# Optimization experiments

Measured on AMD Instinct MI355X. Metric: run time of the kernel, lower is better.

The kernel has to match this reference:

```python
import jax, jax.numpy as jnp
import numpy as np

B, C, H, W, K = 4, 64, 128, 128, 3
K2 = K * K
PAD = (K - 1) // 2  # same padding for 3x3


def setup_inputs() -> dict:
    key = jax.random.key(0)
    ks = jax.random.split(key, 9)
    s = 0.05
    return {
        "x": jax.random.normal(ks[0], (B, C, H, W), jnp.float32),
        "inter": jax.random.normal(ks[1], (B, C, H, W), jnp.float32),
        # offset/mask predictor conv: input cat([x, inter]) -> 3*K2 channels (dy, dx, mask)
        "w_offset": jax.random.normal(ks[2], (3 * K2, 2 * C, K, K), jnp.float32) * s,
        "b_offset": jnp.zeros((3 * K2,), jnp.float32),
        # deformable conv weight (bias=False per DGM init)
        "w_dcn": jax.random.normal(ks[3], (C, C, K, K), jnp.float32) * s,
        # SFT gamma branch: two 1x1 convs (bias=False)
        "w_g1": jax.random.normal(ks[4], (C, C), jnp.float32) * s,
        "w_g2": jax.random.normal(ks[5], (C, C), jnp.float32) * s,
        # SFT beta branch: two 1x1 convs (bias=False)
        "w_b1": jax.random.normal(ks[6], (C, C), jnp.float32) * s,
        "w_b2": jax.random.normal(ks[7], (C, C), jnp.float32) * s,
    }


def _lrelu(v):
    # LeakyReLU(0.1)
    return jnp.where(v >= 0, v, 0.1 * v)


def _conv(x, w, b=None):
    y = jax.lax.conv_general_dilated(
        x, w, window_strides=(1, 1), padding=[(PAD, PAD), (PAD, PAD)],
        dimension_numbers=("NCHW", "OIHW", "NCHW"))
    if b is not None:
        y = y + b[None, :, None, None]
    return y


def _bilinear_gather(x, py, px):
    """x: [B,C,H,W]; py, px: [B,K2,H,W] float sample coords.
    Returns samples [B,K2,H,W,C]; out-of-bounds treated as zero (DCN zero-pad)."""
    y0 = jnp.floor(py)
    x0 = jnp.floor(px)
    wy = (py - y0)[..., None]
    wx = (px - x0)[..., None]

    def gather(yi, xi):
        valid = ((yi >= 0) & (yi < H) & (xi >= 0) & (xi < W)).astype(x.dtype)
        yc = jnp.clip(yi, 0, H - 1).astype(jnp.int32)
        xc = jnp.clip(xi, 0, W - 1).astype(jnp.int32)
        bidx = jnp.arange(B)[:, None, None, None]
        v = x[bidx, :, yc, xc]  # advanced indexing -> [B,K2,H,W,C]
        return v * valid[..., None]

    v00 = gather(y0, x0)
    v01 = gather(y0, x0 + 1)
    v10 = gather(y0 + 1, x0)
    v11 = gather(y0 + 1, x0 + 1)
    return (v00 * (1 - wy) * (1 - wx) + v01 * (1 - wy) * wx
            + v10 * wy * (1 - wx) + v11 * wy * wx)


def _dgm_forward(x, inter, w_offset, b_offset, w_dcn, w_g1, w_g2, w_b1, w_b2):
    # --- WADCN branch: modulated deformable conv, offsets predicted from cat(x, inter)
    om = _conv(jnp.concatenate([x, inter], axis=1), w_offset, b_offset)  # [B,3K2,H,W]
    dy, dx, m = jnp.split(om, 3, axis=1)  # each [B,K2,H,W]
    mask = jax.nn.sigmoid(m)

    ky, kx = jnp.meshgrid(jnp.arange(K), jnp.arange(K), indexing="ij")
    ky = ky.reshape(K2).astype(x.dtype)
    kx = kx.reshape(K2).astype(x.dtype)
    hh = jnp.arange(H, dtype=x.dtype)
    ww = jnp.arange(W, dtype=x.dtype)
    # sample coords: base grid + kernel-tap offset + learned offset
    py = hh[None, None, :, None] + (ky - PAD)[None, :, None, None] + dy  # [B,K2,H,W]
    px = ww[None, None, None, :] + (kx - PAD)[None, :, None, None] + dx

    samp = _bilinear_gather(x, py, px) * mask[..., None]  # [B,K2,H,W,C]
    dcn_out = jnp.einsum("bkhwc,ock->bohw", samp, w_dcn.reshape(C, C, K2))

    # --- SFT branch: two 1x1-conv + LeakyReLU chains producing gamma/beta
    gamma = jnp.einsum("oc,bchw->bohw", w_g2,
                       _lrelu(jnp.einsum("oc,bchw->bohw", w_g1, inter)))
    beta = jnp.einsum("oc,bchw->bohw", w_b2,
                      _lrelu(jnp.einsum("oc,bchw->bohw", w_b1, inter)))
    sft_out = x * gamma + beta

    # --- fused residual combine (DGM.relu is defined but never applied)
    return x + dcn_out + sft_out


def reference(x, inter, w_offset, b_offset, w_dcn, w_g1, w_g2, w_b1, w_b2):
    return _dgm_forward(x, inter, w_offset, b_offset, w_dcn, w_g1, w_g2, w_b1, w_b2)
```

## Files before the change

kernel.cpp:

```cpp
#include <hip/hip_runtime.h>
#include <hip/hip_bf16.h>
#include <math.h>

#define BB 4
#define CC 64
#define HH 128
#define WW 128
#define HW (HH*WW)
#define NPIX (BB*HW)

typedef __attribute__((ext_vector_type(8))) short short8;
typedef __attribute__((ext_vector_type(4))) float f32x4;

__device__ __forceinline__ float bf2f(ushort u) {
  union { unsigned u; float f; } v; v.u = ((unsigned)u) << 16; return v.f;
}
__device__ __forceinline__ ushort f2bf(float f) {
  __hip_bfloat16 h = __float2bfloat16(f); return *(ushort*)&h;
}

#define XOFS   0u
#define IOFS   4194304u
#define ZPOFS  12017664u

__global__ __launch_bounds__(256) void k_transp(
    const float* __restrict__ x, const float* __restrict__ inter,
    ushort* __restrict__ x_clh, ushort* __restrict__ inter_clh) {
  __shared__ float tile[64 * 129];
  int blk = blockIdx.x;
  int sel = blk >> 9;
  int bh = blk & 511;
  int b = bh >> 7, h = bh & 127;
  const float* src = sel ? inter : x;
  ushort* dst = sel ? inter_clh : x_clh;
  const float* sp = src + (size_t)(b * 64) * HW + h * WW;
  for (int i = threadIdx.x; i < 64 * 128; i += 256) {
    int c = i >> 7, w = i & 127;
    tile[c * 129 + w] = sp[(size_t)c * HW + w];
  }
  __syncthreads();
  ushort* dp = dst + ((size_t)b * HW + h * WW) * 64;
  for (int i = threadIdx.x; i < 64 * 128; i += 256) {
    int w = i >> 6, c = i & 63;
    dp[w * 64 + c] = f2bf(tile[c * 129 + w]);
  }
}

__global__ void k_wprep(const float* __restrict__ w_off,
                        const float* __restrict__ w_dcn,
                        const float* __restrict__ wg1, const float* __restrict__ wb1,
                        const float* __restrict__ wg2, const float* __restrict__ wb2,
                        ushort* __restrict__ wfb, ushort* __restrict__ wdT,
                        ushort* __restrict__ w1gb, ushort* __restrict__ w1bb,
                        ushort* __restrict__ w2gb, ushort* __restrict__ w2bb,
                        float* __restrict__ zp) {
  int blk = blockIdx.x;
  if (blk < 144) {
    int i = blk * 256 + threadIdx.x;
    if (i < 64) zp[i] = 0.f;
    if (i < 9 * 32 * 128) {
      int tap = i >> 12, rem = i & 4095, m = rem >> 7, c = rem & 127;
      float v = (m < 27) ? w_off[(size_t)(m * 128 + c) * 9 + tap] : 0.f;
      wfb[i] = f2bf(v);
    }
  } else if (blk < 288) {
    int i = (blk - 144) * 256 + threadIdx.x;
    if (i < 64 * 64 * 9) {
      int o = i / 576, rem = i % 576, k = rem >> 6, c = rem & 63;
      wdT[i] = f2bf(w_dcn[(o * 64 + c) * 9 + k]);
    }
  } else {
    int i = (blk - 288) * 256 + threadIdx.x;
    int m = i >> 12, j = i & 4095;
    const float* src = (m == 0) ? wg1 : (m == 1) ? wb1 : (m == 2) ? wg2 : wb2;
    ushort* dst = (m == 0) ? w1gb : (m == 1) ? w1bb : (m == 2) ? w2gb : w2bb;
    dst[j] = f2bf(src[j]);
  }
}

#define FPITCH 72

__global__ __launch_bounds__(256) void k_sft(
    const float* __restrict__ x, const ushort* __restrict__ inter_clh,
    const ushort* __restrict__ w1gb, const ushort* __restrict__ w1bb,
    const ushort* __restrict__ w2gb, const ushort* __restrict__ w2bb,
    float* __restrict__ out) {
  __shared__ ushort Sg[64 * FPITCH];
  __shared__ ushort Sb[64 * FPITCH];
  int tid = threadIdx.x;
  int lane = tid & 63;
  int quad = lane >> 4, col = lane & 15;
  int pg0 = blockIdx.x * 64;
  int b = pg0 >> 14, hw0 = pg0 & 16383;
  int o_base = __builtin_amdgcn_readfirstlane((tid >> 6) * 16);

  f32x4 ag[4], ab[4];
#pragma unroll
  for (int nt = 0; nt < 4; ++nt) {
    ag[nt] = (f32x4){0.f, 0.f, 0.f, 0.f};
    ab[nt] = (f32x4){0.f, 0.f, 0.f, 0.f};
  }
#pragma unroll
  for (int ks = 0; ks < 2; ++ks) {
    short8 a_g = *(const short8*)(w1gb + (size_t)(o_base + col) * 64 + ks * 32 + quad * 8);
    short8 a_b = *(const short8*)(w1bb + (size_t)(o_base + col) * 64 + ks * 32 + quad * 8);
#pragma unroll
    for (int nt = 0; nt < 4; ++nt) {
      short8 bf = *(const short8*)(inter_clh + (size_t)(pg0 + nt * 16 + col) * 64 + ks * 32 + quad * 8);
      ag[nt] = __builtin_amdgcn_mfma_f32_16x16x32_bf16(a_g, bf, ag[nt], 0, 0, 0);
      ab[nt] = __builtin_amdgcn_mfma_f32_16x16x32_bf16(a_b, bf, ab[nt], 0, 0, 0);
    }
  }
#pragma unroll
  for (int nt = 0; nt < 4; ++nt) {
    int px = nt * 16 + col;
    ushort pkg[4], pkb[4];
#pragma unroll
    for (int r = 0; r < 4; ++r) {
      float vg = ag[nt][r]; vg = vg >= 0.f ? vg : 0.1f * vg;
      float vb = ab[nt][r]; vb = vb >= 0.f ? vb : 0.1f * vb;
      pkg[r] = f2bf(vg); pkb[r] = f2bf(vb);
    }
    *(uint2*)(&Sg[px * FPITCH + o_base + quad * 4]) = *(uint2*)pkg;
    *(uint2*)(&Sb[px * FPITCH + o_base + quad * 4]) = *(uint2*)pkb;
  }
  __syncthreads();

  f32x4 gg[4], gb[4];
#pragma unroll
  for (int nt = 0; nt < 4; ++nt) {
    gg[nt] = (f32x4){0.f, 0.f, 0.f, 0.f};
    gb[nt] = (f32x4){0.f, 0.f, 0.f, 0.f};
  }
#pragma unroll
  for (int ks = 0; ks < 2; ++ks) {
    short8 a_g = *(const short8*)(w2gb + (size_t)(o_base + col) * 64 + ks * 32 + quad * 8);
    short8 a_b = *(const short8*)(w2bb + (size_t)(o_base + col) * 64 + ks * 32 + quad * 8);
#pragma unroll
    for (int nt = 0; nt < 4; ++nt) {
      short8 bg = *(const short8*)(Sg + (nt * 16 + col) * FPITCH + ks * 32 + quad * 8);
      short8 bb = *(const short8*)(Sb + (nt * 16 + col) * FPITCH + ks * 32 + quad * 8);
      gg[nt] = __builtin_amdgcn_mfma_f32_16x16x32_bf16(a_g, bg, gg[nt], 0, 0, 0);
      gb[nt] = __builtin_amdgcn_mfma_f32_16x16x32_bf16(a_b, bb, gb[nt], 0, 0, 0);
    }
  }

#pragma unroll
  for (int nt = 0; nt < 4; ++nt) {
#pragma unroll
    for (int r = 0; r < 4; ++r) {
      int o = o_base + quad * 4 + r;
      size_t idx = (size_t)(b * 64 + o) * HW + hw0 + nt * 16 + col;
      float xv = x[idx];
      out[idx] = xv + xv * gg[nt][r] + gb[nt][r];
    }
  }
}

__global__ __launch_bounds__(256, 2) void k_convm(
    const ushort* __restrict__ wsb, const ushort* __restrict__ wfb,
    float* __restrict__ om) {
  int tid = threadIdx.x;
  int wave = tid >> 6, lane = tid & 63;
  int quad = lane >> 4, col = lane & 15;
  int blk = blockIdx.x;
  int b = blk >> 7, h = blk & 127;
  int half = wave >> 1, mt = wave & 1;

  short8 A[36];
  {
    const ushort* wb0 = wfb + (size_t)(mt * 16 + col) * 128 + quad * 8;
#pragma unroll
    for (int tap = 0; tap < 9; ++tap)
#pragma unroll
      for (int g = 0; g < 2; ++g)
#pragma unroll
        for (int ks = 0; ks < 2; ++ks)
          A[tap * 4 + g * 2 + ks] =
              *(const short8*)(wb0 + (size_t)tap * 4096 + g * 64 + ks * 32);
  }

  unsigned bslab = (unsigned)b * HW * 64;
  int pgrow = b * HW + h * WW;

#pragma unroll 1
  for (int t = 0; t < 4; ++t) {
    int px = half * 64 + t * 16 + col;
    unsigned ofs[9];
#pragma unroll
    for (int ky = 0; ky < 3; ++ky) {
      int hs = h + ky - 1;
      bool hok = (unsigned)hs < 128u;
#pragma unroll
      for (int kx = 0; kx < 3; ++kx) {
        int ps = px + kx - 1;
        bool ok = hok && ((unsigned)ps < 128u);
        unsigned o = bslab + (unsigned)((hs << 7) + ps) * 64 + quad * 8;
        ofs[ky * 3 + kx] = ok ? o : ZPOFS;
      }
    }
    f32x4 accx = {0.f, 0.f, 0.f, 0.f}, acci = {0.f, 0.f, 0.f, 0.f};
#pragma unroll
    for (int tap = 0; tap < 9; ++tap) {
      const ushort* p = wsb + ofs[tap];
      short8 bx0 = *(const short8*)(p + XOFS);
      short8 bx1 = *(const short8*)(p + XOFS + 32);
      short8 bi0 = *(const short8*)(p + IOFS);
      short8 bi1 = *(const short8*)(p + IOFS + 32);
      accx = __builtin_amdgcn_mfma_f32_16x16x32_bf16(A[tap * 4 + 0], bx0, accx, 0, 0, 0);
      accx = __builtin_amdgcn_mfma_f32_16x16x32_bf16(A[tap * 4 + 1], bx1, accx, 0, 0, 0);
      acci = __builtin_amdgcn_mfma_f32_16x16x32_bf16(A[tap * 4 + 2], bi0, acci, 0, 0, 0);
      acci = __builtin_amdgcn_mfma_f32_16x16x32_bf16(A[tap * 4 + 3], bi1, acci, 0, 0, 0);
    }
    int pg = pgrow + px;
#pragma unroll
    for (int r = 0; r < 4; ++r) {
      int o = mt * 16 + quad * 4 + r;
      float v = accx[r] + acci[r];
      if (o < 27) om[(size_t)o * NPIX + pg] = v;
    }
  }
}

#define SPITCH 200
#define NPX 32

__global__ __launch_bounds__(256) void k_dcn(
    const ushort* __restrict__ x_clh, const float* __restrict__ om,
    const float* __restrict__ b_off, const ushort* __restrict__ wdT,
    const ushort* __restrict__ zp16,
    float* __restrict__ out) {
  __shared__ ushort S[NPX * SPITCH];
  __shared__ int   cy[9 * NPX], cx[9 * NPX];
  __shared__ float cwy[9 * NPX], cwx[9 * NPX], cm[9 * NPX];

  int tid = threadIdx.x;
  int wave = tid >> 6, lane = tid & 63;
  int quad = lane >> 4, col = lane & 15;
  int rr = lane >> 3, g = lane & 7;
  int pg0 = blockIdx.x * NPX;
  int b = pg0 >> 14;
  int o_base = __builtin_amdgcn_readfirstlane(wave * 16);

  for (int i = tid; i < 9 * NPX; i += 256) {
    int k = i >> 5, p = i & 31;
    int pg = pg0 + p;
    int hw = pg & 16383;
    int h = hw >> 7, w = hw & 127;
    float dy = om[(size_t)k * NPIX + pg] + b_off[k];
    float dx = om[(size_t)(9 + k) * NPIX + pg] + b_off[9 + k];
    float mz = om[(size_t)(18 + k) * NPIX + pg] + b_off[18 + k];
    float py = (float)(h + (k / 3) - 1) + dy;
    float px = (float)(w + (k % 3) - 1) + dx;
    float y0f = floorf(py), x0f = floorf(px);
    cy[i] = (int)y0f;
    cx[i] = (int)x0f;
    cwy[i] = py - y0f;
    cwx[i] = px - x0f;
    cm[i] = 1.f / (1.f + __expf(-mz));
  }

  f32x4 acc[2];
  acc[0] = (f32x4){0.f, 0.f, 0.f, 0.f};
  acc[1] = (f32x4){0.f, 0.f, 0.f, 0.f};

  const ushort* bp = x_clh + (size_t)b * HW * 64;

  for (int chunk = 0; chunk < 3; ++chunk) {
    __syncthreads();
#pragma unroll
    for (int it = 0; it < 3; ++it) {
      int p = wave * 8 + rr;
      int idx = (chunk * 3 + it) * NPX + p;
      int y0 = cy[idx], x0 = cx[idx];
      float wy = cwy[idx], wx = cwx[idx], m = cm[idx];
      bool yok0 = (unsigned)y0 < 128u, yok1 = (unsigned)(y0 + 1) < 128u;
      bool xok0 = (unsigned)x0 < 128u, xok1 = (unsigned)(x0 + 1) < 128u;
      const ushort* r0 = bp + ((size_t)(int)((y0 << 7) + x0)) * 64 + g * 8;
      const ushort* r1 = r0 + (size_t)WW * 64;
      short8 s00 = *(const short8*)((yok0 && xok0) ? r0 : zp16);
      short8 s01 = *(const short8*)((yok0 && xok1) ? (r0 + 64) : zp16);
      short8 s10 = *(const short8*)((yok1 && xok0) ? r1 : zp16);
      short8 s11 = *(const short8*)((yok1 && xok1) ? (r1 + 64) : zp16);
      short8 outv;
#pragma unroll
      for (int j = 0; j < 8; ++j) {
        float v00 = bf2f((ushort)s00[j]), v01 = bf2f((ushort)s01[j]);
        float v10 = bf2f((ushort)s10[j]), v11 = bf2f((ushort)s11[j]);
        float top = v00 + (v01 - v00) * wx;
        float bot = v10 + (v11 - v10) * wx;
        float val = top + (bot - top) * wy;
        outv[j] = (short)f2bf(val * m);
      }
      *(short8*)(&S[p * SPITCH + it * 64 + g * 8]) = outv;
    }
    __syncthreads();
    const ushort* wrow = wdT + (size_t)(o_base + col) * 576 + chunk * 192 + quad * 8;
    const ushort* srow = S + quad * 8;
#pragma unroll
    for (int ks = 0; ks < 6; ++ks) {
      short8 a = *(const short8*)(wrow + ks * 32);
#pragma unroll
      for (int nt = 0; nt < 2; ++nt) {
        short8 bf = *(const short8*)(srow + (nt * 16 + col) * SPITCH + ks * 32);
        acc[nt] = __builtin_amdgcn_mfma_f32_16x16x32_bf16(a, bf, acc[nt], 0, 0, 0);
      }
    }
  }

  int hw0 = pg0 & 16383;
#pragma unroll
  for (int nt = 0; nt < 2; ++nt) {
#pragma unroll
    for (int r = 0; r < 4; ++r) {
      int o = o_base + quad * 4 + r;
      size_t idx = (size_t)(b * 64 + o) * HW + hw0 + nt * 16 + col;
      out[idx] += acc[nt][r];
    }
  }
}

extern "C" void kernel_launch(void* const* d_in, const int* in_sizes, int n_in,
                              void* d_out, int out_size, void* d_ws, size_t ws_size,
                              hipStream_t stream) {
  const float* x     = (const float*)d_in[0];
  const float* inter = (const float*)d_in[1];
  const float* w_off = (const float*)d_in[2];
  const float* b_off = (const float*)d_in[3];
  const float* w_dcn = (const float*)d_in[4];
  const float* wg1   = (const float*)d_in[5];
  const float* wg2   = (const float*)d_in[6];
  const float* wb1   = (const float*)d_in[7];
  const float* wb2   = (const float*)d_in[8];
  float* out = (float*)d_out;

  float* ws        = (float*)d_ws;
  ushort* wsb      = (ushort*)d_ws;
  ushort* x_clh    = (ushort*)ws;
  ushort* inter_clh= (ushort*)(ws + 2097152);
  float* om        = ws + 4194304;
  ushort* wfb      = (ushort*)(ws + 5963776);
  ushort* wdT      = (ushort*)(ws + 5982208);
  ushort* w1gb     = (ushort*)(ws + 6000640);
  ushort* w1bb     = (ushort*)(ws + 6002688);
  ushort* w2gb     = (ushort*)(ws + 6004736);
  ushort* w2bb     = (ushort*)(ws + 6006784);
  float* zp        = ws + 6008832;

  k_transp<<<1024, 256, 0, stream>>>(x, inter, x_clh, inter_clh);
  k_wprep<<<352, 256, 0, stream>>>(w_off, w_dcn, wg1, wb1, wg2, wb2,
                                   wfb, wdT, w1gb, w1bb, w2gb, w2bb, zp);

  k_sft<<<1024, 256, 0, stream>>>(x, inter_clh, w1gb, w1bb, w2gb, w2bb, out);

  k_convm<<<512, 256, 0, stream>>>(wsb, wfb, om);

  k_dcn<<<2048, 256, 0, stream>>>(x_clh, om, b_off, wdT, (const ushort*)zp, out);
}
```

Measured before the change: 183.7 us.

## Split offset conv across more blocks and software-pipeline weight and input loads

The offset/mask conv kernel no longer preloads all 36 weight fragments into registers. Instead it streams each tap's weights and inputs, double-buffered one tap ahead. Each block now handles a quarter of an image row (32 pixels), one tile per wave, with 4x as many blocks and launch bounds raised to 4 blocks per CU. This lowers register pressure, raises occupancy and parallelism, and overlaps loads with MFMA. The cost is that weights are re-read from global/L2 for every pixel tile instead of once per block.

Result: slower. 206.6 us (+12.5%).

```diff
diff --git a/kernel.cpp b/kernel.cpp
--- a/kernel.cpp
+++ b/kernel.cpp
@@ -157,68 +157,78 @@
   }
 }
 
-__global__ __launch_bounds__(256, 2) void k_convm(
+__global__ __launch_bounds__(256, 4) void k_convm(
     const ushort* __restrict__ wsb, const ushort* __restrict__ wfb,
     float* __restrict__ om) {
   int tid = threadIdx.x;
   int wave = tid >> 6, lane = tid & 63;
   int quad = lane >> 4, col = lane & 15;
   int blk = blockIdx.x;
-  int b = blk >> 7, h = blk & 127;
-  int half = wave >> 1, mt = wave & 1;
-
-  short8 A[36];
+  int b = blk >> 9, h = (blk >> 2) & 127, wq = blk & 3;
+  int pt = wave >> 1, mt = wave & 1;
+  int px = wq * 32 + pt * 16 + col;
+
+  unsigned bslab = (unsigned)b * HW * 64;
+  unsigned ofsx[9], ofsi[9];
+#pragma unroll
+  for (int ky = 0; ky < 3; ++ky) {
+    int hs = h + ky - 1;
+    bool hok = (unsigned)hs < 128u;
+#pragma unroll
+    for (int kx = 0; kx < 3; ++kx) {
+      int ps = px + kx - 1;
+      bool ok = hok && ((unsigned)ps < 128u);
+      unsigned o = bslab + (unsigned)((hs << 7) + ps) * 64 + quad * 8;
+      ofsx[ky * 3 + kx] = ok ? (XOFS + o) : ZPOFS;
+      ofsi[ky * 3 + kx] = ok ? (IOFS + o) : ZPOFS;
+    }
+  }
+
+  const ushort* wb0 = wfb + (size_t)(mt * 16 + col) * 128 + quad * 8;
+
+  short8 bx0[2], bx1[2], bi0[2], bi1[2], a0[2], a1[2], a2[2], a3[2];
   {
-    const ushort* wb0 = wfb + (size_t)(mt * 16 + col) * 128 + quad * 8;
-#pragma unroll
-    for (int tap = 0; tap < 9; ++tap)
-#pragma unroll
-      for (int g = 0; g < 2; ++g)
-#pragma unroll
-        for (int ks = 0; ks < 2; ++ks)
-          A[tap * 4 + g * 2 + ks] =
-              *(const short8*)(wb0 + (size_t)tap * 4096 + g * 64 + ks * 32);
-  }
-
-  unsigned bslab = (unsigned)b * HW * 64;
-  int pgrow = b * HW + h * WW;
-
-#pragma unroll 1
-  for (int t = 0; t < 4; ++t) {
-    int px = half * 64 + t * 16 + col;
-    unsigned ofs[9];
-#pragma unroll
-    for (int ky = 0; ky < 3; ++ky) {
-      int hs = h + ky - 1;
-      bool hok = (unsigned)hs < 128u;
-#pragma unroll
-      for (int kx = 0; kx < 3; ++kx) {
-        int ps = px + kx - 1;
-        bool ok = hok && ((unsigned)ps < 128u);
-        unsigned o = bslab + (unsigned)((hs << 7) + ps) * 64 + quad * 8;
-        ofs[ky * 3 + kx] = ok ? o : ZPOFS;
-      }
-    }
-    f32x4 accx = {0.f, 0.f, 0.f, 0.f}, acci = {0.f, 0.f, 0.f, 0.f};
-#pragma unroll
-    for (int tap = 0; tap < 9; ++tap) {
-      const ushort* p = wsb + ofs[tap];
-      short8 bx0 = *(const short8*)(p + XOFS);
-      short8 bx1 = *(const short8*)(p + XOFS + 32);
-      short8 bi0 = *(const short8*)(p + IOFS);
-      short8 bi1 = *(const short8*)(p + IOFS + 32);
-      accx = __builtin_amdgcn_mfma_f32_16x16x32_bf16(A[tap * 4 + 0], bx0, accx, 0, 0, 0);
-      accx = __builtin_amdgcn_mfma_f32_16x16x32_bf16(A[tap * 4 + 1], bx1, accx, 0, 0, 0);
-      acci = __builtin_amdgcn_mfma_f32_16x16x32_bf16(A[tap * 4 + 2], bi0, acci, 0, 0, 0);
-      acci = __builtin_amdgcn_mfma_f32_16x16x32_bf16(A[tap * 4 + 3], bi1, acci, 0, 0, 0);
-    }
-    int pg = pgrow + px;
-#pragma unroll
-    for (int r = 0; r < 4; ++r) {
-      int o = mt * 16 + quad * 4 + r;
-      float v = accx[r] + acci[r];
-      if (o < 27) om[(size_t)o * NPIX + pg] = v;
-    }
+    const ushort* pxp = wsb + ofsx[0];
+    const ushort* pip = wsb + ofsi[0];
+    bx0[0] = *(const short8*)(pxp);
+    bx1[0] = *(const short8*)(pxp + 32);
+    bi0[0] = *(const short8*)(pip);
+    bi1[0] = *(const short8*)(pip + 32);
+    a0[0] = *(const short8*)(wb0 + 0);
+    a1[0] = *(const short8*)(wb0 + 32);
+    a2[0] = *(const short8*)(wb0 + 64);
+    a3[0] = *(const short8*)(wb0 + 96);
+  }
+
+  f32x4 accx = {0.f, 0.f, 0.f, 0.f}, acci = {0.f, 0.f, 0.f, 0.f};
+#pragma unroll
+  for (int tap = 0; tap < 9; ++tap) {
+    int cur = tap & 1, nxt = cur ^ 1;
+    if (tap < 8) {
+      const ushort* pxp = wsb + ofsx[tap + 1];
+      const ushort* pip = wsb + ofsi[tap + 1];
+      bx0[nxt] = *(const short8*)(pxp);
+      bx1[nxt] = *(const short8*)(pxp + 32);
+      bi0[nxt] = *(const short8*)(pip);
+      bi1[nxt] = *(const short8*)(pip + 32);
+      const ushort* wt = wb0 + (size_t)(tap + 1) * 4096;
+      a0[nxt] = *(const short8*)(wt + 0);
+      a1[nxt] = *(const short8*)(wt + 32);
+      a2[nxt] = *(const short8*)(wt + 64);
+      a3[nxt] = *(const short8*)(wt + 96);
+    }
+    accx = __builtin_amdgcn_mfma_f32_16x16x32_bf16(a0[cur], bx0[cur], accx, 0, 0, 0);
+    accx = __builtin_amdgcn_mfma_f32_16x16x32_bf16(a1[cur], bx1[cur], accx, 0, 0, 0);
+    acci = __builtin_amdgcn_mfma_f32_16x16x32_bf16(a2[cur], bi0[cur], acci, 0, 0, 0);
+    acci = __builtin_amdgcn_mfma_f32_16x16x32_bf16(a3[cur], bi1[cur], acci, 0, 0, 0);
+  }
+
+  int pg = b * HW + h * WW + px;
+#pragma unroll
+  for (int r = 0; r < 4; ++r) {
+    int o = mt * 16 + quad * 4 + r;
+    float v = accx[r] + acci[r];
+    if (o < 27) om[(size_t)o * NPIX + pg] = v;
   }
 }
 
@@ -353,7 +363,7 @@
 
   k_sft<<<1024, 256, 0, stream>>>(x, inter_clh, w1gb, w1bb, w2gb, w2bb, out);
 
-  k_convm<<<512, 256, 0, stream>>>(wsb, wfb, om);
+  k_convm<<<2048, 256, 0, stream>>>(wsb, wfb, om);
 
   k_dcn<<<2048, 256, 0, stream>>>(x_clh, om, b_off, wdT, (const ushort*)zp, out);
 }
```
